# Kernel optimization log

Hardware: AMD Instinct MI355X
Metric: run time of the kernel (lower is better)

The kernel has to match this reference:

```python
import jax, jax.numpy as jnp
import numpy as np

TAU = 0.05
MASK_VAL = -1000000000.0
EPS = 1e-12  # torch F.normalize eps


def _l2norm(x):
    n = jnp.linalg.norm(x, axis=-1, keepdims=True)
    return x / jnp.maximum(n, EPS)


def setup_inputs() -> dict:
    key = jax.random.key(0)
    k1, k2 = jax.random.split(key)
    N, D = 16384, 64
    z1 = jax.random.normal(k1, (N, D), dtype=jnp.float32)
    z2 = jax.random.normal(k2, (N, D), dtype=jnp.float32)
    return {"z1": z1, "z2": z2}


def reference(z1, z2):
    # normalize both views
    z1n = _l2norm(z1)
    z2n = _l2norm(z2)
    N = z1n.shape[0]
    # full similarity matrix [N, N]
    sim = jnp.einsum("nd,md->nm", z1n, z2n) / TAU
    pos = jnp.diagonal(sim)  # sim(z1[i], z2[i]) / tau
    # mask the positive position inside the negatives block (as the torch code does)
    eye = jnp.eye(N, dtype=bool)
    neg = jnp.where(eye, MASK_VAL, sim)
    # logits = [pos, masked row]; label = 0 -> CE = logsumexp(logits) - pos
    logits = jnp.concatenate([pos[:, None], neg], axis=1)  # [N, N+1]
    lse = jax.nn.logsumexp(logits, axis=1)
    loss = jnp.sum(lse - pos) / N
    return loss
```

## Files before the change

kernel.cpp:

```cpp
#include <hip/hip_runtime.h>
#include <hip/hip_bf16.h>


typedef __bf16  bf16x8 __attribute__((ext_vector_type(8)));
typedef float   f32x4  __attribute__((ext_vector_type(4)));

#if __has_builtin(__builtin_amdgcn_exp2f)
#define EXP2F(x) __builtin_amdgcn_exp2f(x)
#else
#define EXP2F(x) exp2f(x)
#endif
#if __has_builtin(__builtin_amdgcn_logf)
#define LOG2F(x) __builtin_amdgcn_logf(x)
#else
#define LOG2F(x) log2f(x)
#endif

#define DDIM   64
#define ROWB   128
#define NW     4
#define WROWS  64
#define BM     (NW * WROWS)
#define CHUNK  64
#define CS     16
#define TILEB  2048
#define BUFB   (4 * TILEB)

__global__ __launch_bounds__(256) void norm_both_kernel(
    const float* __restrict__ z1, const float* __restrict__ z2,
    __hip_bfloat16* __restrict__ out, float scale1, int N)
{
    int gr   = (blockIdx.x * 256 + threadIdx.x) >> 6;
    int lane = threadIdx.x & 63;
    const float* src = (gr < N) ? (z1 + (size_t)gr * DDIM)
                                : (z2 + (size_t)(gr - N) * DDIM);
    float scale = (gr < N) ? scale1 : 1.0f;
    float v  = src[lane];
    float ss = v * v;
    #pragma unroll
    for (int off = 32; off; off >>= 1) ss += __shfl_xor(ss, off);
    float n = fmaxf(sqrtf(ss), 1e-12f);
    out[(size_t)gr * DDIM + lane] = __float2bfloat16((v / n) * scale);
}

__global__ __launch_bounds__(256) void infonce_main_kernel(
    const __hip_bfloat16* __restrict__ z1s,
    const __hip_bfloat16* __restrict__ z2s,
    float* __restrict__ partial,
    float* __restrict__ posv,
    int N)
{
    __shared__ char lds[2 * BUFB];

    const int tid  = threadIdx.x;
    const int wave = tid >> 6;
    const int lane = tid & 63;
    const int q    = lane >> 4;
    const int l15  = lane & 15;

    const int colspan = N / CS;
    const int c0      = blockIdx.y * colspan;
    const int wr      = blockIdx.x * BM + wave * WROWS;

    bf16x8 a0[4], a1[4];
    #pragma unroll
    for (int s = 0; s < 4; ++s) {
        const char* ab = (const char*)z1s + (size_t)(wr + s * 16 + l15) * ROWB + q * 16;
        a0[s] = *(const bf16x8*)(ab);
        a1[s] = *(const bf16x8*)(ab + 64);
    }

    float sum[16];
    #pragma unroll
    for (int k = 0; k < 16; ++k) sum[k] = 0.f;

    const int gsA = tid, gsB = tid + 256;
    const int rowA = ((gsA >> 7) << 4) | (gsA & 15);
    const int rowB = ((gsB >> 7) << 4) | (gsB & 15);
    const int pA = (((gsA & 127) >> 6) << 2) | (((gsA & 127) >> 4) & 3);
    const int pB = (((gsB & 127) >> 6) << 2) | (((gsB & 127) >> 4) & 3);
    const char* z2b = (const char*)z2s;

    *(float4*)(lds + gsA * 16) = *(const float4*)(z2b + (size_t)(c0 + rowA) * ROWB + pA * 16);
    *(float4*)(lds + gsB * 16) = *(const float4*)(z2b + (size_t)(c0 + rowB) * ROWB + pB * 16);
    __syncthreads();

    int pb = 0;
    for (int cc = 0; cc < colspan; cc += CHUNK) {
        float4 vA, vB;
        const bool has_next = (cc + CHUNK) < colspan;
        if (has_next) {
            const int nc = c0 + cc + CHUNK;
            vA = *(const float4*)(z2b + (size_t)(nc + rowA) * ROWB + pA * 16);
            vB = *(const float4*)(z2b + (size_t)(nc + rowB) * ROWB + pB * 16);
        }

        const char* buf = lds + pb * BUFB;
        #pragma unroll
        for (int ct = 0; ct < 4; ++ct) {
            const char* bb = buf + ct * TILEB + lane * 16;
            bf16x8 b0 = *(const bf16x8*)(bb);
            bf16x8 b1 = *(const bf16x8*)(bb + 1024);
            const int cg = c0 + cc + ct * 16;
            #pragma unroll
            for (int s = 0; s < 4; ++s) {
                f32x4 acc = {0.f, 0.f, 0.f, 0.f};
                acc = __builtin_amdgcn_mfma_f32_16x16x32_bf16(a0[s], b0, acc, 0, 0, 0);
                acc = __builtin_amdgcn_mfma_f32_16x16x32_bf16(a1[s], b1, acc, 0, 0, 0);
                if (cg == wr + s * 16) {
                    #pragma unroll
                    for (int i = 0; i < 4; ++i)
                        if (l15 == q * 4 + i) posv[cg + q * 4 + i] = acc[i];
                }
                sum[s * 4 + 0] += EXP2F(acc[0]);
                sum[s * 4 + 1] += EXP2F(acc[1]);
                sum[s * 4 + 2] += EXP2F(acc[2]);
                sum[s * 4 + 3] += EXP2F(acc[3]);
            }
        }

        if (has_next) {
            char* nbuf = lds + (pb ^ 1) * BUFB;
            *(float4*)(nbuf + gsA * 16) = vA;
            *(float4*)(nbuf + gsB * 16) = vB;
        }
        __syncthreads();
        pb ^= 1;
    }

    #pragma unroll
    for (int k = 0; k < 16; ++k) {
        float v = sum[k];
        #pragma unroll
        for (int off = 1; off < 16; off <<= 1) v += __shfl_xor(v, off);
        sum[k] = v;
    }
    if (l15 == 0) {
        float* dst = partial + (size_t)blockIdx.y * N + wr;
        #pragma unroll
        for (int s = 0; s < 4; ++s)
            #pragma unroll
            for (int i = 0; i < 4; ++i)
                dst[s * 16 + q * 4 + i] = sum[s * 4 + i];
    }
}

__global__ __launch_bounds__(256) void finalize_kernel(
    const float* __restrict__ partial, const float* __restrict__ posv,
    float* __restrict__ out, int N)
{
    int row = blockIdx.x * 256 + threadIdx.x;
    float s = 0.f;
    #pragma unroll
    for (int c = 0; c < CS; ++c) s += partial[(size_t)c * N + row];
    float acc = (LOG2F(s) - posv[row]) * (0.69314718055994531f / (float)N);
    #pragma unroll
    for (int off = 32; off; off >>= 1) acc += __shfl_xor(acc, off);
    if ((threadIdx.x & 63) == 0) atomicAdd(out, acc);
}

extern "C" void kernel_launch(void* const* d_in, const int* in_sizes, int n_in,
                              void* d_out, int out_size, void* d_ws, size_t ws_size,
                              hipStream_t stream)
{
    const float* z1 = (const float*)d_in[0];
    const float* z2 = (const float*)d_in[1];
    const int N = in_sizes[0] / DDIM;

    char* ws = (char*)d_ws;
    __hip_bfloat16* z1s = (__hip_bfloat16*)ws;
    __hip_bfloat16* z2s = z1s + (size_t)N * DDIM;
    float* partial = (float*)(ws + 2 * (size_t)N * ROWB);
    float* posv    = partial + (size_t)CS * N;

    const float kScale = 28.853900817779268f;

    hipMemsetAsync(d_out, 0, sizeof(float), stream);

    norm_both_kernel<<<2 * N / 4, 256, 0, stream>>>(z1, z2, z1s, kScale, N);

    dim3 grid(N / BM, CS);
    infonce_main_kernel<<<grid, NW * 64, 0, stream>>>(z1s, z2s, partial, posv, N);

    finalize_kernel<<<N / 256, 256, 0, stream>>>(partial, posv, (float*)d_out, N);
}
```

Measured before the change: 128.4 us.

## Pre-swizzle normalized inputs into MFMA fragment layout and drop LDS staging

The normalize kernel now writes z1/z2 in bf16 directly in the 16x16x32 MFMA fragment order, so the main kernel loads B fragments straight from global memory without LDS double-buffering or barriers. Column splits go from 16 to 32, and per-row partial sums are combined with atomics into a single rowsum array instead of a CS-by-N partial buffer. The output memset is folded into the normalize kernel. This removes LDS traffic and syncs and the separate memset, at the cost of every wave reading B from L2/global directly, with no sharing among the four waves of a block, plus more atomics.

```diff
diff --git a/kernel.cpp b/kernel.cpp
--- a/kernel.cpp
+++ b/kernel.cpp
@@ -3,6 +3,7 @@
 
 
 typedef __bf16  bf16x8 __attribute__((ext_vector_type(8)));
+typedef __bf16  bf16x4 __attribute__((ext_vector_type(4)));
 typedef float   f32x4  __attribute__((ext_vector_type(4)));
 
 #if __has_builtin(__builtin_amdgcn_exp2f)
@@ -17,41 +18,58 @@
 #endif
 
 #define DDIM   64
-#define ROWB   128
+#define TILEB  2048
+#define NSETS  4
 #define NW     4
-#define WROWS  64
-#define BM     (NW * WROWS)
-#define CHUNK  64
-#define CS     16
-#define TILEB  2048
-#define BUFB   (4 * TILEB)
+#define BM     (NW * NSETS * 16)
+#define CS     32
 
-__global__ __launch_bounds__(256) void norm_both_kernel(
+__global__ __launch_bounds__(256) void norm_frag_kernel(
     const float* __restrict__ z1, const float* __restrict__ z2,
-    __hip_bfloat16* __restrict__ out, float scale1, int N)
+    __hip_bfloat16* __restrict__ z1f, __hip_bfloat16* __restrict__ z2f,
+    float* __restrict__ rowsum, float* __restrict__ out,
+    float scale1, int N)
 {
-    int gr   = (blockIdx.x * 256 + threadIdx.x) >> 6;
-    int lane = threadIdx.x & 63;
-    const float* src = (gr < N) ? (z1 + (size_t)gr * DDIM)
-                                : (z2 + (size_t)(gr - N) * DDIM);
-    float scale = (gr < N) ? scale1 : 1.0f;
-    float v  = src[lane];
-    float ss = v * v;
-    #pragma unroll
-    for (int off = 32; off; off >>= 1) ss += __shfl_xor(ss, off);
-    float n = fmaxf(sqrtf(ss), 1e-12f);
-    out[(size_t)gr * DDIM + lane] = __float2bfloat16((v / n) * scale);
+    const int tid  = threadIdx.x;
+    const int r    = tid >> 4, c = tid & 15;
+    const int tile = blockIdx.x;
+    const size_t row = (size_t)tile * 16 + r;
+    const size_t off = (size_t)tile * TILEB
+                     + ((c >> 3) << 10) + (((c >> 1) & 3) << 8)
+                     + (r << 4) + ((c & 1) << 3);
+
+    {
+        float4 v = *(const float4*)(z1 + row * DDIM + c * 4);
+        float ss = v.x*v.x + v.y*v.y + v.z*v.z + v.w*v.w;
+        #pragma unroll
+        for (int o = 8; o; o >>= 1) ss += __shfl_xor(ss, o);
+        float inv = scale1 / fmaxf(sqrtf(ss), 1e-12f);
+        bf16x4 ov = { __float2bfloat16(v.x*inv), __float2bfloat16(v.y*inv),
+                      __float2bfloat16(v.z*inv), __float2bfloat16(v.w*inv) };
+        *(bf16x4*)((char*)z1f + off) = ov;
+    }
+    {
+        float4 v = *(const float4*)(z2 + row * DDIM + c * 4);
+        float ss = v.x*v.x + v.y*v.y + v.z*v.z + v.w*v.w;
+        #pragma unroll
+        for (int o = 8; o; o >>= 1) ss += __shfl_xor(ss, o);
+        float inv = 1.0f / fmaxf(sqrtf(ss), 1e-12f);
+        bf16x4 ov = { __float2bfloat16(v.x*inv), __float2bfloat16(v.y*inv),
+                      __float2bfloat16(v.z*inv), __float2bfloat16(v.w*inv) };
+        *(bf16x4*)((char*)z2f + off) = ov;
+    }
+
+    if (tid < 16) rowsum[(size_t)tile * 16 + tid] = 0.f;
+    if (tile == 0 && tid == 0) *out = 0.f;
 }
 
 __global__ __launch_bounds__(256) void infonce_main_kernel(
-    const __hip_bfloat16* __restrict__ z1s,
-    const __hip_bfloat16* __restrict__ z2s,
-    float* __restrict__ partial,
+    const __hip_bfloat16* __restrict__ z1f,
+    const __hip_bfloat16* __restrict__ z2f,
+    float* __restrict__ rowsum,
     float* __restrict__ posv,
     int N)
 {
-    __shared__ char lds[2 * BUFB];
-
     const int tid  = threadIdx.x;
     const int wave = tid >> 6;
     const int lane = tid & 63;
@@ -60,102 +78,70 @@
 
     const int colspan = N / CS;
     const int c0      = blockIdx.y * colspan;
-    const int wr      = blockIdx.x * BM + wave * WROWS;
+    const int wr      = blockIdx.x * BM + wave * (NSETS * 16);
 
-    bf16x8 a0[4], a1[4];
+    bf16x8 a0[NSETS], a1[NSETS];
     #pragma unroll
-    for (int s = 0; s < 4; ++s) {
-        const char* ab = (const char*)z1s + (size_t)(wr + s * 16 + l15) * ROWB + q * 16;
+    for (int s = 0; s < NSETS; ++s) {
+        const char* ab = (const char*)z1f + (size_t)((wr >> 4) + s) * TILEB + lane * 16;
         a0[s] = *(const bf16x8*)(ab);
-        a1[s] = *(const bf16x8*)(ab + 64);
+        a1[s] = *(const bf16x8*)(ab + 1024);
     }
 
-    float sum[16];
+    float sum[NSETS * 4];
     #pragma unroll
-    for (int k = 0; k < 16; ++k) sum[k] = 0.f;
+    for (int k = 0; k < NSETS * 4; ++k) sum[k] = 0.f;
 
-    const int gsA = tid, gsB = tid + 256;
-    const int rowA = ((gsA >> 7) << 4) | (gsA & 15);
-    const int rowB = ((gsB >> 7) << 4) | (gsB & 15);
-    const int pA = (((gsA & 127) >> 6) << 2) | (((gsA & 127) >> 4) & 3);
-    const int pB = (((gsB & 127) >> 6) << 2) | (((gsB & 127) >> 4) & 3);
-    const char* z2b = (const char*)z2s;
+    const char* bptr = (const char*)z2f + (size_t)(c0 >> 4) * TILEB + lane * 16;
+    const int ntiles = colspan >> 4;
 
-    *(float4*)(lds + gsA * 16) = *(const float4*)(z2b + (size_t)(c0 + rowA) * ROWB + pA * 16);
-    *(float4*)(lds + gsB * 16) = *(const float4*)(z2b + (size_t)(c0 + rowB) * ROWB + pB * 16);
-    __syncthreads();
-
-    int pb = 0;
-    for (int cc = 0; cc < colspan; cc += CHUNK) {
-        float4 vA, vB;
-        const bool has_next = (cc + CHUNK) < colspan;
-        if (has_next) {
-            const int nc = c0 + cc + CHUNK;
-            vA = *(const float4*)(z2b + (size_t)(nc + rowA) * ROWB + pA * 16);
-            vB = *(const float4*)(z2b + (size_t)(nc + rowB) * ROWB + pB * 16);
+    #pragma unroll 2
+    for (int t = 0; t < ntiles; ++t) {
+        bf16x8 b0 = *(const bf16x8*)(bptr);
+        bf16x8 b1 = *(const bf16x8*)(bptr + 1024);
+        bptr += TILEB;
+        const int cg = c0 + (t << 4);
+        #pragma unroll
+        for (int s = 0; s < NSETS; ++s) {
+            f32x4 acc = {0.f, 0.f, 0.f, 0.f};
+            acc = __builtin_amdgcn_mfma_f32_16x16x32_bf16(a0[s], b0, acc, 0, 0, 0);
+            acc = __builtin_amdgcn_mfma_f32_16x16x32_bf16(a1[s], b1, acc, 0, 0, 0);
+            if (cg == wr + s * 16) {
+                #pragma unroll
+                for (int i = 0; i < 4; ++i)
+                    if (l15 == q * 4 + i) posv[cg + q * 4 + i] = acc[i];
+            }
+            sum[s * 4 + 0] += EXP2F(acc[0]);
+            sum[s * 4 + 1] += EXP2F(acc[1]);
+            sum[s * 4 + 2] += EXP2F(acc[2]);
+            sum[s * 4 + 3] += EXP2F(acc[3]);
         }
-
-        const char* buf = lds + pb * BUFB;
-        #pragma unroll
-        for (int ct = 0; ct < 4; ++ct) {
-            const char* bb = buf + ct * TILEB + lane * 16;
-            bf16x8 b0 = *(const bf16x8*)(bb);
-            bf16x8 b1 = *(const bf16x8*)(bb + 1024);
-            const int cg = c0 + cc + ct * 16;
-            #pragma unroll
-            for (int s = 0; s < 4; ++s) {
-                f32x4 acc = {0.f, 0.f, 0.f, 0.f};
-                acc = __builtin_amdgcn_mfma_f32_16x16x32_bf16(a0[s], b0, acc, 0, 0, 0);
-                acc = __builtin_amdgcn_mfma_f32_16x16x32_bf16(a1[s], b1, acc, 0, 0, 0);
-                if (cg == wr + s * 16) {
-                    #pragma unroll
-                    for (int i = 0; i < 4; ++i)
-                        if (l15 == q * 4 + i) posv[cg + q * 4 + i] = acc[i];
-                }
-                sum[s * 4 + 0] += EXP2F(acc[0]);
-                sum[s * 4 + 1] += EXP2F(acc[1]);
-                sum[s * 4 + 2] += EXP2F(acc[2]);
-                sum[s * 4 + 3] += EXP2F(acc[3]);
-            }
-        }
-
-        if (has_next) {
-            char* nbuf = lds + (pb ^ 1) * BUFB;
-            *(float4*)(nbuf + gsA * 16) = vA;
-            *(float4*)(nbuf + gsB * 16) = vB;
-        }
-        __syncthreads();
-        pb ^= 1;
     }
 
     #pragma unroll
-    for (int k = 0; k < 16; ++k) {
+    for (int k = 0; k < NSETS * 4; ++k) {
         float v = sum[k];
         #pragma unroll
-        for (int off = 1; off < 16; off <<= 1) v += __shfl_xor(v, off);
+        for (int o = 1; o < 16; o <<= 1) v += __shfl_xor(v, o);
         sum[k] = v;
     }
     if (l15 == 0) {
-        float* dst = partial + (size_t)blockIdx.y * N + wr;
         #pragma unroll
-        for (int s = 0; s < 4; ++s)
+        for (int s = 0; s < NSETS; ++s)
             #pragma unroll
             for (int i = 0; i < 4; ++i)
-                dst[s * 16 + q * 4 + i] = sum[s * 4 + i];
+                atomicAdd(&rowsum[wr + s * 16 + q * 4 + i], sum[s * 4 + i]);
     }
 }
 
 __global__ __launch_bounds__(256) void finalize_kernel(
-    const float* __restrict__ partial, const float* __restrict__ posv,
+    const float* __restrict__ rowsum, const float* __restrict__ posv,
     float* __restrict__ out, int N)
 {
     int row = blockIdx.x * 256 + threadIdx.x;
-    float s = 0.f;
+    float acc = (LOG2F(rowsum[row]) - posv[row]) * (0.69314718055994531f / (float)N);
     #pragma unroll
-    for (int c = 0; c < CS; ++c) s += partial[(size_t)c * N + row];
-    float acc = (LOG2F(s) - posv[row]) * (0.69314718055994531f / (float)N);
-    #pragma unroll
-    for (int off = 32; off; off >>= 1) acc += __shfl_xor(acc, off);
+    for (int o = 32; o; o >>= 1) acc += __shfl_xor(acc, o);
     if ((threadIdx.x & 63) == 0) atomicAdd(out, acc);
 }
 
@@ -168,19 +154,18 @@
     const int N = in_sizes[0] / DDIM;
 
     char* ws = (char*)d_ws;
-    __hip_bfloat16* z1s = (__hip_bfloat16*)ws;
-    __hip_bfloat16* z2s = z1s + (size_t)N * DDIM;
-    float* partial = (float*)(ws + 2 * (size_t)N * ROWB);
-    float* posv    = partial + (size_t)CS * N;
+    __hip_bfloat16* z1f = (__hip_bfloat16*)ws;
+    __hip_bfloat16* z2f = z1f + (size_t)N * DDIM;
+    float* rowsum = (float*)(ws + 2 * (size_t)N * DDIM * 2);
+    float* posv   = rowsum + N;
 
     const float kScale = 28.853900817779268f;
 
-    hipMemsetAsync(d_out, 0, sizeof(float), stream);
-
-    norm_both_kernel<<<2 * N / 4, 256, 0, stream>>>(z1, z2, z1s, kScale, N);
+    norm_frag_kernel<<<N / 16, 256, 0, stream>>>(z1, z2, z1f, z2f, rowsum,
+                                                 (float*)d_out, kScale, N);
 
     dim3 grid(N / BM, CS);
-    infonce_main_kernel<<<grid, NW * 64, 0, stream>>>(z1s, z2s, partial, posv, N);
+    infonce_main_kernel<<<grid, NW * 64, 0, stream>>>(z1f, z2f, rowsum, posv, N);
 
-    finalize_kernel<<<N / 256, 256, 0, stream>>>(partial, posv, (float*)d_out, N);
+    finalize_kernel<<<N / 256, 256, 0, stream>>>(rowsum, posv, (float*)d_out, N);
 }
```

Result: faster. 115.4 us (-10.2%).
